# Kernel tuning notes

Measured on AMD Instinct MI355X. Metric: run time of the kernel, lower is better.

The kernel has to match this reference:

```python
import jax, jax.numpy as jnp
from jax import lax
import numpy as np

DN = ('NHWC', 'HWIO', 'NHWC')  # NHWC activations, HWIO kernels (TF layout)
EPS = 1e-3


def setup_inputs() -> dict:
    key = jax.random.key(0)
    ks = jax.random.split(key, 6)
    B, H, W, C = 16, 64, 64, 256
    x = jax.random.normal(ks[0], (B, H, W, C), jnp.float32)
    # per-sample predicted kernels (scaled to keep activations well-conditioned)
    depthwise_kernels = jax.random.normal(ks[1], (B, 3, 3, C, C), jnp.float32) * 0.02
    pointwise_kernels = jax.random.normal(ks[2], (B, 1, 1, C, C), jnp.float32) * 0.06
    biases = jax.random.normal(ks[3], (B, C), jnp.float32) * 0.1
    # shared trailing Conv2D layer params
    conv_w = jax.random.normal(ks[4], (3, 3, C, C), jnp.float32) * 0.02
    conv_b = jnp.zeros((C,), jnp.float32)
    return dict(x=x, depthwise_kernels=depthwise_kernels,
                pointwise_kernels=pointwise_kernels, biases=biases,
                conv_w=conv_w, conv_b=conv_b)


def _instance_norm(x):
    # tf.nn.moments over spatial dims (population variance), eps=0.001
    mean = jnp.mean(x, axis=(1, 2), keepdims=True)
    var = jnp.var(x, axis=(1, 2), keepdims=True)
    return (x - mean) * lax.rsqrt(var + EPS)


def _reflect_pad_hw(x, p=1):
    pad = [(0, 0)] * (x.ndim - 3) + [(p, p), (p, p), (0, 0)]
    return jnp.pad(x, pad, mode='reflect')


def _per_sample_conv(xi, dk, pk, bi):
    # xi: [H,W,C]; dk: [3,3,C,Cm]; pk: [1,1,Cm,Co]; bi: [Co]
    xp = _reflect_pad_hw(xi)[None]  # [1,H+2,W+2,C]
    y = lax.conv_general_dilated(xp, dk, (1, 1), 'VALID', dimension_numbers=DN)
    y = lax.conv_general_dilated(y, pk, (1, 1), 'VALID', dimension_numbers=DN)
    return (y + bi)[0]


def reference(x, depthwise_kernels, pointwise_kernels, biases, conv_w, conv_b):
    x = _instance_norm(x)
    # per-sample kernels -> vmap over batch (replaces tf.map_fn)
    x = jax.vmap(_per_sample_conv)(x, depthwise_kernels, pointwise_kernels, biases)
    # shared Conv2D: reflect pad + VALID conv + bias
    xp = _reflect_pad_hw(x)
    y = lax.conv_general_dilated(xp, conv_w, (1, 1), 'VALID', dimension_numbers=DN)
    return y + conv_b
```

## Files before the change

kernel.cpp:

```cpp
#include <hip/hip_runtime.h>


typedef __bf16 bf16x8 __attribute__((ext_vector_type(8)));
typedef float f32x4 __attribute__((ext_vector_type(4)));

__device__ __forceinline__ float bf2f(unsigned short v) {
    return __uint_as_float(((unsigned int)v) << 16);
}
__device__ __forceinline__ unsigned short f2bf(float f) {
    unsigned int u = __float_as_uint(f);
    unsigned int r = (u + 0x7FFFu + ((u >> 16) & 1u)) >> 16;
    return (unsigned short)r;
}
__device__ __forceinline__ float ldg_elem(const void* p, size_t idx, bool isbf) {
    return isbf ? bf2f(((const unsigned short*)p)[idx]) : ((const float*)p)[idx];
}

__device__ __forceinline__ void gload16(const void* g, void* l) {
    __builtin_amdgcn_global_load_lds(
        (__attribute__((address_space(1))) void*)(unsigned long long)g,
        (__attribute__((address_space(3))) void*)(unsigned long long)l,
        16, 0, 0);
}

#define RAW_BARRIER() do { asm volatile("" ::: "memory"); \
                           __builtin_amdgcn_s_barrier();   \
                           asm volatile("" ::: "memory"); } while (0)

__global__ void detect_dtype(const unsigned short* __restrict__ x, int* __restrict__ flag) {
    __shared__ int wild;
    if (threadIdx.x == 0) wild = 0;
    __syncthreads();
    int cnt = 0;
    for (int i = 0; i < 16; ++i) {
        float a = fabsf(bf2f(x[threadIdx.x * 16 + i]));
        if (!(a < 64.f) || (a != 0.f && a < 1e-5f)) cnt++;
    }
    atomicAdd(&wild, cnt);
    __syncthreads();
    if (threadIdx.x == 0) *flag = (wild > 512) ? 0 : 1;
}

__global__ void norm_partial2(const void* __restrict__ x, const int* __restrict__ flag,
                              float* __restrict__ partS, float* __restrict__ partQ) {
    const bool isbf = (*flag != 0);
    const int b = blockIdx.x, ch = blockIdx.y;
    const int t = threadIdx.x;
    const int l = t & 63;
    const int c4 = l * 4;
    const int sp0 = t >> 6;
    const size_t base = ((size_t)(b * 4096 + ch * 128 + sp0)) * 256 + c4;
    float s[4] = {0.f, 0.f, 0.f, 0.f}, q[4] = {0.f, 0.f, 0.f, 0.f};
    if (isbf) {
        for (int i = 0; i < 32; ++i) {
            const unsigned short* p = (const unsigned short*)x + base + (size_t)i * 1024;
            ushort4 v = *(const ushort4*)p;
            float a[4] = {bf2f(v.x), bf2f(v.y), bf2f(v.z), bf2f(v.w)};
#pragma unroll
            for (int j = 0; j < 4; ++j) { s[j] += a[j]; q[j] += a[j] * a[j]; }
        }
    } else {
        for (int i = 0; i < 32; ++i) {
            float4 v = *(const float4*)((const float*)x + base + (size_t)i * 1024);
            float a[4] = {v.x, v.y, v.z, v.w};
#pragma unroll
            for (int j = 0; j < 4; ++j) { s[j] += a[j]; q[j] += a[j] * a[j]; }
        }
    }
    __shared__ float red[4][64][9];
#pragma unroll
    for (int j = 0; j < 4; ++j) { red[sp0][l][j] = s[j]; red[sp0][l][4 + j] = q[j]; }
    __syncthreads();
    if (t < 64) {
#pragma unroll
        for (int j = 0; j < 4; ++j) {
            float ss = red[0][t][j] + red[1][t][j] + red[2][t][j] + red[3][t][j];
            float qq = red[0][t][4 + j] + red[1][t][4 + j] + red[2][t][4 + j] + red[3][t][4 + j];
            int c = t * 4 + j;
            partS[(b * 32 + ch) * 256 + c] = ss;
            partQ[(b * 32 + ch) * 256 + c] = qq;
        }
    }
}

__global__ void norm_finalize2(const float* __restrict__ partS, const float* __restrict__ partQ,
                               float* __restrict__ mean, float* __restrict__ rstd) {
    const int b = blockIdx.x, c = threadIdx.x;
    float s = 0.f, q = 0.f;
    for (int k = 0; k < 32; ++k) {
        s += partS[(b * 32 + k) * 256 + c];
        q += partQ[(b * 32 + k) * 256 + c];
    }
    float m = s * (1.f / 4096.f);
    float v = q * (1.f / 4096.f) - m * m;
    mean[b * 256 + c] = m;
    rstd[b * 256 + c] = rsqrtf(v + 1e-3f);
}

__global__ void norm_apply(const void* __restrict__ x, const int* __restrict__ flag,
                           const float* __restrict__ mean, const float* __restrict__ rstd,
                           unsigned short* __restrict__ xn) {
    const bool isbf = (*flag != 0);
    size_t e = ((size_t)blockIdx.x * 256 + threadIdx.x) * 8;
    int c0 = (int)(e & 255);
    int bc = (int)(e >> 20) * 256 + c0;
    float v[8];
    if (isbf) {
        uint4 raw = *(const uint4*)((const unsigned short*)x + e);
        unsigned int rr[4] = {raw.x, raw.y, raw.z, raw.w};
#pragma unroll
        for (int i = 0; i < 4; ++i) {
            v[2 * i]     = bf2f((unsigned short)(rr[i] & 0xFFFF));
            v[2 * i + 1] = bf2f((unsigned short)(rr[i] >> 16));
        }
    } else {
        float4 f0 = *(const float4*)((const float*)x + e);
        float4 f1 = *(const float4*)((const float*)x + e + 4);
        v[0] = f0.x; v[1] = f0.y; v[2] = f0.z; v[3] = f0.w;
        v[4] = f1.x; v[5] = f1.y; v[6] = f1.z; v[7] = f1.w;
    }
    unsigned int o[4];
#pragma unroll
    for (int i = 0; i < 4; ++i) {
        unsigned short lo = f2bf((v[2 * i]     - mean[bc + 2 * i])     * rstd[bc + 2 * i]);
        unsigned short hi = f2bf((v[2 * i + 1] - mean[bc + 2 * i + 1]) * rstd[bc + 2 * i + 1]);
        o[i] = (unsigned int)lo | ((unsigned int)hi << 16);
    }
    uint4 out; out.x = o[0]; out.y = o[1]; out.z = o[2]; out.w = o[3];
    *(uint4*)(xn + e) = out;
}

template <bool SCALE>
__global__ void transpose_wk(const void* __restrict__ src, const int* __restrict__ flag,
                             unsigned short* __restrict__ dst,
                             int s_per, long dstBStride, int coStride,
                             const float* __restrict__ rstd) {
    __shared__ unsigned short tile[64][66];
    const bool isbf = (*flag != 0);
    const int sl = blockIdx.x;
    const int b = sl / s_per;
    const size_t dbase = (size_t)b * (size_t)dstBStride + (size_t)(sl % s_per) * 256;
    const int ci0 = blockIdx.y * 64, co0 = blockIdx.z * 64;
    const int t = threadIdx.x;
    const int co4 = (t & 15) * 4;
    const int r0 = t >> 4;
#pragma unroll
    for (int i = 0; i < 4; ++i) {
        int r = r0 + i * 16;
        size_t sidx = (size_t)sl * 65536 + (size_t)(ci0 + r) * 256 + co0 + co4;
        if (isbf) {
            ushort4 v = *(const ushort4*)((const unsigned short*)src + sidx);
            tile[r][co4] = v.x; tile[r][co4 + 1] = v.y;
            tile[r][co4 + 2] = v.z; tile[r][co4 + 3] = v.w;
        } else {
            float4 v = *(const float4*)((const float*)src + sidx);
            tile[r][co4] = f2bf(v.x); tile[r][co4 + 1] = f2bf(v.y);
            tile[r][co4 + 2] = f2bf(v.z); tile[r][co4 + 3] = f2bf(v.w);
        }
    }
    __syncthreads();
    const int cip = (t & 31) * 2;
    const int cob = t >> 5;
    float s0 = 1.f, s1 = 1.f;
    if (SCALE) { s0 = rstd[b * 256 + ci0 + cip]; s1 = rstd[b * 256 + ci0 + cip + 1]; }
#pragma unroll
    for (int i = 0; i < 8; ++i) {
        int co = cob + i * 8;
        unsigned short lo = tile[cip][co], hi = tile[cip + 1][co];
        if (SCALE) { lo = f2bf(bf2f(lo) * s0); hi = f2bf(bf2f(hi) * s1); }
        *(unsigned int*)(dst + dbase + (size_t)(co0 + co) * coStride + ci0 + cip) =
            (unsigned int)lo | ((unsigned int)hi << 16);
    }
}

__global__ void corr_kernel(const unsigned short* __restrict__ dkT,
                            const float* __restrict__ mean,
                            float* __restrict__ negcorr) {
    const int b = blockIdx.x;
    const int lane = threadIdx.x & 63;
    const int co = blockIdx.y * 4 + (threadIdx.x >> 6);
    const unsigned short* wp = dkT + (size_t)(b * 256 + co) * 2304;
    const float* mb = mean + b * 256;
    const int ci0 = (lane & 31) * 8;
    float4 ma = *(const float4*)(mb + ci0);
    float4 mc = *(const float4*)(mb + ci0 + 4);
    float mm[8] = {ma.x, ma.y, ma.z, ma.w, mc.x, mc.y, mc.z, mc.w};
    float sum = 0.f;
#pragma unroll
    for (int c = 0; c < 5; ++c) {
        int k = c * 512 + lane * 8;
        if (k < 2304) {
            uint4 w = *(const uint4*)(wp + k);
            unsigned int wsv[4] = {w.x, w.y, w.z, w.w};
#pragma unroll
            for (int j = 0; j < 4; ++j) {
                sum += bf2f((unsigned short)(wsv[j] & 0xFFFF)) * mm[2 * j];
                sum += bf2f((unsigned short)(wsv[j] >> 16)) * mm[2 * j + 1];
            }
        }
    }
#pragma unroll
    for (int off = 32; off > 0; off >>= 1) sum += __shfl_down(sum, off);
    if (lane == 0) negcorr[b * 256 + co] = -sum;
}

template <bool PER_SAMPLE_W, int BIAS_MODE, bool OUT_F32>
__global__ __launch_bounds__(512, 2) void conv3x3_256(const unsigned short* __restrict__ src,
                                                      const int* __restrict__ flag,
                                                      const unsigned short* __restrict__ wT,
                                                      const void* __restrict__ bias,
                                                      void* __restrict__ dst) {
    constexpr int KTOT = 2304;
    extern __shared__ unsigned short smem[];

    const int t = threadIdx.x;
    const int lane = t & 63;
    const int wave = t >> 6;
    const int wr = wave >> 1;
    const int wc = wave & 1;
    const int bid = blockIdx.x + 16 * blockIdx.z;
    const int b  = (bid & 7) + ((bid >> 3) & 1) * 8;
    const int mt = bid >> 4;
    const int m0 = mt * 256;
    const int R0 = mt * 4;
    const unsigned short* srcB = src + (size_t)b * (4096 * 256);
    const unsigned short* wB = wT + (PER_SAMPLE_W ? (size_t)b * 256 * KTOT : (size_t)0);
    const bool in_bf = (BIAS_MODE >= 2) ? (*flag != 0) : true;

    const int wx = t >> 3;
    const int wg = ((t & 7) ^ (wx & 7)) << 3;
    int wrow[6];
#pragma unroll
    for (int u = 0; u < 6; ++u) {
        int r = R0 - 1 + u;
        wrow[u] = (r < 0) ? 1 : (r > 63 ? 62 : r);
    }
    const unsigned short* winsrc[6];
#pragma unroll
    for (int u = 0; u < 6; ++u)
        winsrc[u] = srcB + ((size_t)wrow[u] * 64 + wx) * 256 + wg;

    const int btrow = t >> 2;
    const int bg = ((t & 3) ^ (btrow & 3)) << 3;
    const unsigned short* bsrc = wB + (size_t)btrow * KTOT + bg;

    auto issueB = [&](int jn) {
        const int cgn = jn / 18, scn = jn % 18;
        const int koff = (scn >> 1) * 256 + cgn * 64 + (scn & 1) * 32;
        unsigned short* bdst = smem + 49152 + (jn % 3) * 8192 + wave * 512;
        gload16(bsrc + koff, bdst);
        gload16(bsrc + (size_t)128 * KTOT + koff, bdst + 4096);
    };

    f32x4 acc[4][8];
#pragma unroll
    for (int i = 0; i < 4; ++i)
#pragma unroll
        for (int j = 0; j < 8; ++j) acc[i][j] = (f32x4){0.f, 0.f, 0.f, 0.f};

    const int fr = lane & 15;
    const int quad = lane >> 4;
    const int cn = wc * 128;
    const int bxor = (quad ^ ((cn + fr) & 3)) << 3;
    int boff[8];
#pragma unroll
    for (int n = 0; n < 8; ++n) boff[n] = (cn + n * 16 + fr) * 32 + bxor;

    auto readB = [&](int jn, int n) -> bf16x8 {
        const unsigned short* slotb = smem + 49152 + (jn % 3) * 8192;
        return *(const bf16x8*)(slotb + boff[n]);
    };
    auto readA = [&](int jn, int mi) -> bf16x8 {
        const int cgn = jn / 18, scn = jn % 18;
        const int tap = scn >> 1, half = scn & 1;
        const int dh = tap / 3 - 1, dw = tap % 3 - 1;
        const unsigned short* A1 = smem + (cgn & 1) * 24576 + (wr + 1 + dh) * 4096;
        int ww = mi * 16 + fr + dw;
        ww = (ww < 0) ? 1 : (ww > 63 ? 62 : ww);
        return *(const bf16x8*)(A1 + ww * 64 + (((half * 4 + quad) ^ (ww & 7)) << 3));
    };

#pragma unroll
    for (int u = 0; u < 6; ++u)
        gload16(winsrc[u], smem + u * 4096 + wave * 512);
    issueB(0);
    issueB(1);
    asm volatile("s_waitcnt vmcnt(0)" ::: "memory");
    RAW_BARRIER();

    bf16x8 afA[4], afB[4], bfr[8];
#pragma unroll
    for (int mi = 0; mi < 4; ++mi) afA[mi] = readA(0, mi);
#pragma unroll
    for (int n = 0; n < 8; ++n) bfr[n] = readB(0, n);

    auto step = [&](int j, bf16x8 (&afc)[4], bf16x8 (&afn)[4]) {
        const int jm = j - 1;
        const bool keep1 = (jm >= 0) && ((jm % 18) >= 8) && ((jm % 18) <= 13) && (jm < 54);
        if (keep1) asm volatile("s_waitcnt vmcnt(1)" ::: "memory");
        else       asm volatile("s_waitcnt vmcnt(0)" ::: "memory");
        RAW_BARRIER();

        const int cgj = j / 18, scj = j % 18;
        if (j + 2 < 72) issueB(j + 2);
        if (cgj < 3 && scj >= 8 && scj <= 13) {
            const int u = scj - 8;
            gload16(winsrc[u] + (cgj + 1) * 64,
                    smem + ((cgj + 1) & 1) * 24576 + u * 4096 + wave * 512);
        }
        if (scj == 0 && j > 0) {
#pragma unroll
            for (int mi = 0; mi < 4; ++mi) afc[mi] = readA(j, mi);
        }
        const bool rdnext = (j < 71);
        __builtin_amdgcn_s_setprio(1);
#pragma unroll
        for (int n = 0; n < 8; ++n) {
#pragma unroll
            for (int mi = 0; mi < 4; ++mi)
                acc[mi][n] = __builtin_amdgcn_mfma_f32_16x16x32_bf16(afc[mi], bfr[n], acc[mi][n], 0, 0, 0);
            if (rdnext) bfr[n] = readB(j + 1, n);
        }
        __builtin_amdgcn_s_setprio(0);
        if (rdnext && ((j + 1) % 18 != 0)) {
#pragma unroll
            for (int mi = 0; mi < 4; ++mi) afn[mi] = readA(j + 1, mi);
        }
    };

    for (int jj = 0; jj < 72; jj += 2) {
        step(jj, afA, afB);
        step(jj + 1, afB, afA);
    }

    const int rbase = quad * 4;
    float bv[8];
#pragma unroll
    for (int n = 0; n < 8; ++n) {
        int nn = cn + n * 16 + fr;
        if (BIAS_MODE == 2)      bv[n] = ldg_elem(bias, b * 256 + nn, in_bf);
        else if (BIAS_MODE == 3) bv[n] = ldg_elem(bias, nn, in_bf);
        else                     bv[n] = 0.f;
    }
#pragma unroll
    for (int m = 0; m < 4; ++m) {
#pragma unroll
        for (int rr = 0; rr < 4; ++rr) {
            int mm = m0 + wr * 64 + m * 16 + rbase + rr;
            size_t rowoff = ((size_t)b * 4096 + mm) * 256;
#pragma unroll
            for (int n = 0; n < 8; ++n) {
                int nn = cn + n * 16 + fr;
                float val = acc[m][n][rr] + bv[n];
                if (OUT_F32) ((float*)dst)[rowoff + nn] = val;
                else         ((unsigned short*)dst)[rowoff + nn] = f2bf(val);
            }
        }
    }
}

template <int KSLICES, bool PER_SAMPLE_W, int BIAS_MODE, bool IS3X3, bool OUT_F32>
__global__ __launch_bounds__(512, 2) void gemm_conv_256(const unsigned short* __restrict__ src,
                                                        const int* __restrict__ flag,
                                                        const unsigned short* __restrict__ wT,
                                                        const void* __restrict__ bias,
                                                        void* __restrict__ dst) {
    constexpr int KTOT = KSLICES * 256;
    constexpr int NKT = KTOT / 64;
    static_assert(NKT >= 2, "pipeline needs >=2 K-tiles");
    extern __shared__ unsigned short smem[];

    const int t = threadIdx.x;
    const int lane = t & 63;
    const int wave = t >> 6;
    const int wr = wave >> 2;
    const int wc = wave & 3;
    const int bid = blockIdx.x + 16 * blockIdx.z;
    const int b  = (bid & 7) + ((bid >> 3) & 1) * 8;
    const int m0 = (bid >> 4) * 256;
    const unsigned short* srcB = src + (size_t)b * (4096 * 256);
    const unsigned short* wB = wT + (PER_SAMPLE_W ? (size_t)b * 256 * KTOT : (size_t)0);
    const bool in_bf = (BIAS_MODE >= 2) ? (*flag != 0) : true;

    const int trow = t >> 3;
    const int tswz = ((t & 7) ^ (trow & 7)) << 3;
    int hU[4], wU[4];
#pragma unroll
    for (int u = 0; u < 4; ++u) {
        int m = m0 + u * 64 + trow;
        hU[u] = m >> 6; wU[u] = m & 63;
    }
    const unsigned short* gBu[4];
#pragma unroll
    for (int u = 0; u < 4; ++u)
        gBu[u] = wB + (size_t)(u * 64 + trow) * KTOT + tswz;

    f32x4 acc[8][4];
#pragma unroll
    for (int i = 0; i < 8; ++i)
#pragma unroll
        for (int j = 0; j < 4; ++j) acc[i][j] = (f32x4){0.f, 0.f, 0.f, 0.f};

    const int fr = lane & 15;
    const int quad = lane >> 4;
    const int fsw = fr & 7;
    const int ks0 = ((quad) ^ fsw) << 3;
    const int ks1 = ((quad + 4) ^ fsw) << 3;
    const int rm = wr * 128;
    const int cn = wc * 64;

#pragma unroll
    for (int kt = 0; kt < 2; ++kt) {
        const int pdh = IS3X3 ? -1 : 0;
        const int pdw = IS3X3 ? -1 : 0;
        const int pchb = (kt & 3) << 6;
        unsigned short* ldsAW = smem + kt * 32768 + wave * 512;
#pragma unroll
        for (int u = 0; u < 4; ++u) {
            int hh = hU[u] + pdh; hh = (hh < 0) ? 1 : (hh > 63 ? 62 : hh);
            int ww = wU[u] + pdw; ww = (ww < 0) ? 1 : (ww > 63 ? 62 : ww);
            gload16(srcB + (size_t)((hh << 6) + ww) * 256 + pchb + tswz, ldsAW + u * 4096);
        }
#pragma unroll
        for (int u = 0; u < 4; ++u)
            gload16(gBu[u] + (size_t)kt * 64, ldsAW + 16384 + u * 4096);
    }
    asm volatile("s_waitcnt vmcnt(8)" ::: "memory");
    RAW_BARRIER();

    bf16x8 af[4][2], bfr[4][2];
    size_t aoff[4];
    int cur_s = -1;

    for (int i = 0; i < NKT; ++i) {
        const int buf = i & 1;
        const unsigned short* As_b = smem + buf * 32768;
        const unsigned short* Bs_b = As_b + 16384;
        unsigned short* ldsAW = smem + buf * 32768 + wave * 512;
        const int kt2 = i + 2;
        const bool st = (kt2 < NKT);

#pragma unroll
        for (int m = 0; m < 4; ++m) {
            const unsigned short* rp = As_b + (rm + m * 16 + fr) * 64;
            af[m][0] = *(const bf16x8*)(rp + ks0);
            af[m][1] = *(const bf16x8*)(rp + ks1);
        }
#pragma unroll
        for (int n = 0; n < 2; ++n) {
            const unsigned short* rp = Bs_b + (cn + n * 16 + fr) * 64;
            bfr[n][0] = *(const bf16x8*)(rp + ks0);
            bfr[n][1] = *(const bf16x8*)(rp + ks1);
        }
        __builtin_amdgcn_s_setprio(1);
#pragma unroll
        for (int m = 0; m < 4; ++m)
#pragma unroll
            for (int n = 0; n < 2; ++n) {
                acc[m][n] = __builtin_amdgcn_mfma_f32_16x16x32_bf16(af[m][0], bfr[n][0], acc[m][n], 0, 0, 0);
                acc[m][n] = __builtin_amdgcn_mfma_f32_16x16x32_bf16(af[m][1], bfr[n][1], acc[m][n], 0, 0, 0);
            }
        __builtin_amdgcn_s_setprio(0);

#pragma unroll
        for (int n = 2; n < 4; ++n) {
            const unsigned short* rp = Bs_b + (cn + n * 16 + fr) * 64;
            bfr[n][0] = *(const bf16x8*)(rp + ks0);
            bfr[n][1] = *(const bf16x8*)(rp + ks1);
        }
        __builtin_amdgcn_s_setprio(1);
#pragma unroll
        for (int m = 0; m < 4; ++m)
#pragma unroll
            for (int n = 2; n < 4; ++n) {
                acc[m][n] = __builtin_amdgcn_mfma_f32_16x16x32_bf16(af[m][0], bfr[n][0], acc[m][n], 0, 0, 0);
                acc[m][n] = __builtin_amdgcn_mfma_f32_16x16x32_bf16(af[m][1], bfr[n][1], acc[m][n], 0, 0, 0);
            }
        __builtin_amdgcn_s_setprio(0);

#pragma unroll
        for (int m = 0; m < 4; ++m) {
            const unsigned short* rp = As_b + (rm + 64 + m * 16 + fr) * 64;
            af[m][0] = *(const bf16x8*)(rp + ks0);
            af[m][1] = *(const bf16x8*)(rp + ks1);
        }
        __builtin_amdgcn_s_setprio(1);
#pragma unroll
        for (int m = 0; m < 4; ++m)
#pragma unroll
            for (int n = 0; n < 4; ++n) {
                acc[4 + m][n] = __builtin_amdgcn_mfma_f32_16x16x32_bf16(af[m][0], bfr[n][0], acc[4 + m][n], 0, 0, 0);
                acc[4 + m][n] = __builtin_amdgcn_mfma_f32_16x16x32_bf16(af[m][1], bfr[n][1], acc[4 + m][n], 0, 0, 0);
            }
        __builtin_amdgcn_s_setprio(0);

        RAW_BARRIER();
        if (st) {
            if (IS3X3) {
                const int s2 = kt2 >> 2;
                if (s2 != cur_s) {
                    cur_s = s2;
                    const int dh2 = s2 / 3 - 1, dw2 = s2 % 3 - 1;
#pragma unroll
                    for (int u = 0; u < 4; ++u) {
                        int hh = hU[u] + dh2; hh = (hh < 0) ? 1 : (hh > 63 ? 62 : hh);
                        int ww = wU[u] + dw2; ww = (ww < 0) ? 1 : (ww > 63 ? 62 : ww);
                        aoff[u] = (size_t)((hh << 6) + ww) * 256 + tswz;
                    }
                }
            } else if (cur_s < 0) {
                cur_s = 0;
#pragma unroll
                for (int u = 0; u < 4; ++u)
                    aoff[u] = (size_t)((hU[u] << 6) + wU[u]) * 256 + tswz;
            }
            const int chb2 = (kt2 & 3) << 6;
#pragma unroll
            for (int u = 0; u < 4; ++u)
                gload16(srcB + aoff[u] + chb2, ldsAW + u * 4096);
#pragma unroll
            for (int u = 0; u < 4; ++u)
                gload16(gBu[u] + (size_t)kt2 * 64, ldsAW + 16384 + u * 4096);
            asm volatile("s_waitcnt vmcnt(8)" ::: "memory");
        } else if (i + 1 < NKT) {
            asm volatile("s_waitcnt vmcnt(0)" ::: "memory");
        }
        RAW_BARRIER();
    }

    const int rbase = quad * 4;
    float bv[4];
#pragma unroll
    for (int n = 0; n < 4; ++n) {
        int nn = cn + n * 16 + fr;
        if (BIAS_MODE == 2)      bv[n] = ldg_elem(bias, b * 256 + nn, in_bf);
        else if (BIAS_MODE == 3) bv[n] = ldg_elem(bias, nn, in_bf);
        else                     bv[n] = 0.f;
    }
#pragma unroll
    for (int m = 0; m < 8; ++m) {
#pragma unroll
        for (int rr = 0; rr < 4; ++rr) {
            int mm = m0 + rm + m * 16 + rbase + rr;
            size_t rowoff = ((size_t)b * 4096 + mm) * 256;
#pragma unroll
            for (int n = 0; n < 4; ++n) {
                int nn = cn + n * 16 + fr;
                float val = acc[m][n][rr] + bv[n];
                if (OUT_F32) ((float*)dst)[rowoff + nn] = val;
                else         ((unsigned short*)dst)[rowoff + nn] = f2bf(val);
            }
        }
    }
}

template <int KSLICES, bool PER_SAMPLE_W, int BIAS_MODE, bool IS3X3, bool SRC_ADAPT, bool OUT_F32>
__global__ __launch_bounds__(256) void gemm_conv(const void* __restrict__ src,
                                                 const int* __restrict__ flag,
                                                 const unsigned short* __restrict__ wT,
                                                 const void* __restrict__ bias,
                                                 void* __restrict__ dst) {
    constexpr int KTOT = KSLICES * 256;
    __shared__ unsigned short As[128][40];
    __shared__ unsigned short Bs[128][40];

    const bool in_bf = (SRC_ADAPT || BIAS_MODE >= 2) ? (*flag != 0) : true;
    const int t = threadIdx.x;
    const int b = blockIdx.z;
    const int m0 = blockIdx.x * 128;
    const int n0 = blockIdx.y * 128;
    const size_t srcOfs = (size_t)b * (4096 * 256);
    const unsigned short* wB = wT + (PER_SAMPLE_W ? (size_t)b * 256 * KTOT : (size_t)0);

    f32x4 acc[4][4];
#pragma unroll
    for (int i = 0; i < 4; ++i)
#pragma unroll
        for (int j = 0; j < 4; ++j) acc[i][j] = (f32x4){0.f, 0.f, 0.f, 0.f};

    const int lane = t & 63;
    const int wave = t >> 6;
    const int rm = (wave >> 1) * 64;
    const int cn = (wave & 1) * 64;
    const int fr = lane & 15;
    const int kg = (lane >> 4) * 8;

    for (int kk = 0; kk < KTOT / 32; ++kk) {
        const int k0 = kk * 32;
        const int s = k0 >> 8;
        const int ci0 = k0 & 255;
        const int dh = IS3X3 ? (s / 3) - 1 : 0;
        const int dw = IS3X3 ? (s % 3) - 1 : 0;
        __syncthreads();
#pragma unroll
        for (int cc = 0; cc < 2; ++cc) {
            int ch = t + cc * 256;
            int r = ch >> 2;
            int ko = (ch & 3) << 3;
            int m = m0 + r;
            int h = m >> 6, w = m & 63;
            if (IS3X3) {
                h += dh; h = (h < 0) ? 1 : (h > 63 ? 62 : h);
                w += dw; w = (w < 0) ? 1 : (w > 63 ? 62 : w);
            }
            size_t eidx = srcOfs + (size_t)((h << 6) + w) * 256 + ci0 + ko;
            if (!SRC_ADAPT || in_bf) {
                uint4 v = *(const uint4*)((const unsigned short*)src + eidx);
                *(uint4*)&As[r][ko] = v;
            } else {
                const float* sf = (const float*)src + eidx;
                float4 f0 = *(const float4*)sf;
                float4 f1 = *(const float4*)(sf + 4);
                uint4 v;
                v.x = (unsigned int)f2bf(f0.x) | ((unsigned int)f2bf(f0.y) << 16);
                v.y = (unsigned int)f2bf(f0.z) | ((unsigned int)f2bf(f0.w) << 16);
                v.z = (unsigned int)f2bf(f1.x) | ((unsigned int)f2bf(f1.y) << 16);
                v.w = (unsigned int)f2bf(f1.z) | ((unsigned int)f2bf(f1.w) << 16);
                *(uint4*)&As[r][ko] = v;
            }
        }
#pragma unroll
        for (int cc = 0; cc < 2; ++cc) {
            int ch = t + cc * 256;
            int n = ch >> 2;
            int ko = (ch & 3) << 3;
            uint4 v = *(const uint4*)(wB + (size_t)(n0 + n) * KTOT + k0 + ko);
            *(uint4*)&Bs[n][ko] = v;
        }
        __syncthreads();

        bf16x8 af[4], bfr[4];
#pragma unroll
        for (int i = 0; i < 4; ++i) af[i] = *(const bf16x8*)&As[rm + i * 16 + fr][kg];
#pragma unroll
        for (int j = 0; j < 4; ++j) bfr[j] = *(const bf16x8*)&Bs[cn + j * 16 + fr][kg];
#pragma unroll
        for (int i = 0; i < 4; ++i)
#pragma unroll
            for (int j = 0; j < 4; ++j)
                acc[i][j] = __builtin_amdgcn_mfma_f32_16x16x32_bf16(af[i], bfr[j], acc[i][j], 0, 0, 0);
    }

    const int rbase = (lane >> 4) * 4;
    const int col = lane & 15;
    float bv[4];
#pragma unroll
    for (int j = 0; j < 4; ++j) {
        int n = n0 + cn + j * 16 + col;
        if (BIAS_MODE == 1)      bv[j] = ((const float*)bias)[b * 256 + n];
        else if (BIAS_MODE == 2) bv[j] = ldg_elem(bias, b * 256 + n, in_bf);
        else if (BIAS_MODE == 3) bv[j] = ldg_elem(bias, n, in_bf);
        else                     bv[j] = 0.f;
    }
#pragma unroll
    for (int i = 0; i < 4; ++i) {
#pragma unroll
        for (int rr = 0; rr < 4; ++rr) {
            int m = m0 + rm + i * 16 + rbase + rr;
            size_t rowoff = ((size_t)b * 4096 + m) * 256;
#pragma unroll
            for (int j = 0; j < 4; ++j) {
                int n = n0 + cn + j * 16 + col;
                float val = acc[i][j][rr] + bv[j];
                if (OUT_F32) ((float*)dst)[rowoff + n] = val;
                else         ((unsigned short*)dst)[rowoff + n] = f2bf(val);
            }
        }
    }
}

extern "C" void kernel_launch(void* const* d_in, const int* in_sizes, int n_in,
                              void* d_out, int out_size, void* d_ws, size_t ws_size,
                              hipStream_t stream) {
    const void* x    = d_in[0];
    const void* dk   = d_in[1];
    const void* pk   = d_in[2];
    const void* bias = d_in[3];
    const void* cw   = d_in[4];
    const void* cb   = d_in[5];

    const size_t NEED_SMALL = 36896768u;
    const size_t NEED_BIG   = 55771136u;
    if (ws_size < NEED_SMALL) return;
    const bool big = (ws_size >= NEED_BIG);

    char* ws = (char*)d_ws;
    int*   flagp   = (int*)ws;
    float* meanp   = (float*)(ws + 1024);
    float* rstdp   = (float*)(ws + 17408);
    float* negcorr = (float*)(ws + 33792);
    unsigned short* pkT = (unsigned short*)(ws + 65536);
    unsigned short* cwT = (unsigned short*)(ws + 2162688);
    unsigned short* dkT = (unsigned short*)(ws + 3342336);
    unsigned short* xn  = (unsigned short*)(ws + 22216704);
    float* partS = (float*)(ws + 22216704);
    float* partQ = (float*)(ws + 22216704 + 524288);
    unsigned short* y2  = big ? xn : dkT;
    unsigned short* y1  = (unsigned short*)d_out;

    hipFuncSetAttribute(reinterpret_cast<const void*>(conv3x3_256<true, 0, false>),
                        hipFuncAttributeMaxDynamicSharedMemorySize, 147456);
    hipFuncSetAttribute(reinterpret_cast<const void*>(conv3x3_256<false, 3, true>),
                        hipFuncAttributeMaxDynamicSharedMemorySize, 147456);
    hipFuncSetAttribute(reinterpret_cast<const void*>(gemm_conv_256<1, true, 2, false, false>),
                        hipFuncAttributeMaxDynamicSharedMemorySize, 131072);

    detect_dtype<<<1, 256, 0, stream>>>((const unsigned short*)x, flagp);
    norm_partial2<<<dim3(16, 32), 256, 0, stream>>>(x, flagp, partS, partQ);
    norm_finalize2<<<16, 256, 0, stream>>>(partS, partQ, meanp, rstdp);

    transpose_wk<false><<<dim3(16, 4, 4), 256, 0, stream>>>(pk, flagp, pkT, 1, 65536L, 256, nullptr);
    transpose_wk<false><<<dim3(9, 4, 4), 256, 0, stream>>>(cw, flagp, cwT, 9, 0L, 2304, nullptr);

    if (big) {
        transpose_wk<false><<<dim3(144, 4, 4), 256, 0, stream>>>(dk, flagp, dkT, 9, 589824L, 2304, nullptr);
        norm_apply<<<8192, 256, 0, stream>>>(x, flagp, meanp, rstdp, xn);
        conv3x3_256<true, 0, false><<<dim3(16, 1, 16), 512, 147456, stream>>>(xn, flagp, dkT, nullptr, y1);
    } else {
        transpose_wk<true><<<dim3(144, 4, 4), 256, 0, stream>>>(dk, flagp, dkT, 9, 589824L, 2304, rstdp);
        corr_kernel<<<dim3(16, 64), 256, 0, stream>>>(dkT, meanp, negcorr);
        gemm_conv<9, true, 1, true, true, false><<<dim3(32, 2, 16), 256, 0, stream>>>(x, flagp, dkT, negcorr, y1);
    }

    gemm_conv_256<1, true, 2, false, false><<<dim3(16, 1, 16), 512, 131072, stream>>>(y1, flagp, pkT, bias, y2);
    conv3x3_256<false, 3, true><<<dim3(16, 1, 16), 512, 147456, stream>>>(y2, flagp, cwT, cb, d_out);
}
```

Before: 351.9 us.

## Restructure conv GEMM main loop with single-buffered A window and 64-K B tiles

Replaces the double-buffered A input window (prefetched during the previous channel group) with a single A buffer that is reloaded synchronously at each channel-group boundary. B weight tiles now cover 64 K values per tap in a 3-slot ring, with half issued on each of two half-steps. The MFMA loop moves from an unrolled two-step lambda with interleaved B reads to a plain loop that runs all MFMAs, then reads the next fragments, then does a full vmcnt(0) wait and barrier every step. This simplifies the code and frees LDS, but it exposes A-load latency at group boundaries and removes the interleaving of LDS reads with MFMAs.

```diff
diff --git a/kernel.cpp b/kernel.cpp
--- a/kernel.cpp
+++ b/kernel.cpp
@@ -239,17 +239,13 @@
 #pragma unroll
     for (int u = 0; u < 6; ++u)
         winsrc[u] = srcB + ((size_t)wrow[u] * 64 + wx) * 256 + wg;
-
-    const int btrow = t >> 2;
-    const int bg = ((t & 3) ^ (btrow & 3)) << 3;
-    const unsigned short* bsrc = wB + (size_t)btrow * KTOT + bg;
-
-    auto issueB = [&](int jn) {
-        const int cgn = jn / 18, scn = jn % 18;
-        const int koff = (scn >> 1) * 256 + cgn * 64 + (scn & 1) * 32;
-        unsigned short* bdst = smem + 49152 + (jn % 3) * 8192 + wave * 512;
-        gload16(bsrc + koff, bdst);
-        gload16(bsrc + (size_t)128 * KTOT + koff, bdst + 4096);
+    const unsigned short* bsrc = wB + (size_t)wx * KTOT + wg;
+
+    auto issueB2 = [&](int T, int u0) {
+        const int koff = (T % 9) * 256 + (T / 9) * 64;
+        unsigned short* bdst = smem + 24576 + (T % 3) * 16384 + wave * 512;
+        gload16(bsrc + (size_t)u0 * 64 * KTOT + koff, bdst + u0 * 4096);
+        gload16(bsrc + (size_t)(u0 + 1) * 64 * KTOT + koff, bdst + (u0 + 1) * 4096);
     };
 
     f32x4 acc[4][8];
@@ -261,76 +257,75 @@
     const int fr = lane & 15;
     const int quad = lane >> 4;
     const int cn = wc * 128;
-    const int bxor = (quad ^ ((cn + fr) & 3)) << 3;
-    int boff[8];
-#pragma unroll
-    for (int n = 0; n < 8; ++n) boff[n] = (cn + n * 16 + fr) * 32 + bxor;
 
     auto readB = [&](int jn, int n) -> bf16x8 {
-        const unsigned short* slotb = smem + 49152 + (jn % 3) * 8192;
-        return *(const bf16x8*)(slotb + boff[n]);
+        const int T = jn >> 1, h = jn & 1;
+        const int co = cn + n * 16 + fr;
+        const unsigned short* p = smem + 24576 + (T % 3) * 16384 + co * 64
+                                  + ((((h << 2) + quad) ^ (co & 7)) << 3);
+        return *(const bf16x8*)p;
     };
     auto readA = [&](int jn, int mi) -> bf16x8 {
-        const int cgn = jn / 18, scn = jn % 18;
-        const int tap = scn >> 1, half = scn & 1;
+        const int T = jn >> 1, h = jn & 1;
+        const int tap = T % 9;
         const int dh = tap / 3 - 1, dw = tap % 3 - 1;
-        const unsigned short* A1 = smem + (cgn & 1) * 24576 + (wr + 1 + dh) * 4096;
         int ww = mi * 16 + fr + dw;
         ww = (ww < 0) ? 1 : (ww > 63 ? 62 : ww);
-        return *(const bf16x8*)(A1 + ww * 64 + (((half * 4 + quad) ^ (ww & 7)) << 3));
+        const unsigned short* p = smem + (wr + 1 + dh) * 4096 + ww * 64
+                                  + ((((h << 2) + quad) ^ (ww & 7)) << 3);
+        return *(const bf16x8*)p;
     };
 
 #pragma unroll
     for (int u = 0; u < 6; ++u)
         gload16(winsrc[u], smem + u * 4096 + wave * 512);
-    issueB(0);
-    issueB(1);
+    issueB2(0, 0); issueB2(0, 2);
+    issueB2(1, 0); issueB2(1, 2);
     asm volatile("s_waitcnt vmcnt(0)" ::: "memory");
     RAW_BARRIER();
 
-    bf16x8 afA[4], afB[4], bfr[8];
-#pragma unroll
-    for (int mi = 0; mi < 4; ++mi) afA[mi] = readA(0, mi);
-#pragma unroll
-    for (int n = 0; n < 8; ++n) bfr[n] = readB(0, n);
-
-    auto step = [&](int j, bf16x8 (&afc)[4], bf16x8 (&afn)[4]) {
-        const int jm = j - 1;
-        const bool keep1 = (jm >= 0) && ((jm % 18) >= 8) && ((jm % 18) <= 13) && (jm < 54);
-        if (keep1) asm volatile("s_waitcnt vmcnt(1)" ::: "memory");
-        else       asm volatile("s_waitcnt vmcnt(0)" ::: "memory");
+    bf16x8 afc[4], bfc[8];
+#pragma unroll
+    for (int mi = 0; mi < 4; ++mi) afc[mi] = readA(0, mi);
+#pragma unroll
+    for (int n = 0; n < 8; ++n) bfc[n] = readB(0, n);
+
+    for (int j = 0; j < 72; ++j) {
+        const int T = j >> 1, h = j & 1;
+        const int scj = j % 18;
+
+        if (scj == 0 && j > 0) {
+            const int cgo = (j / 18) * 64;
+#pragma unroll
+            for (int u = 0; u < 6; ++u)
+                gload16(winsrc[u] + cgo, smem + u * 4096 + wave * 512);
+            asm volatile("s_waitcnt vmcnt(0)" ::: "memory");
+            RAW_BARRIER();
+#pragma unroll
+            for (int mi = 0; mi < 4; ++mi) afc[mi] = readA(j, mi);
+        }
+
+        if (T + 2 < 36) issueB2(T + 2, h * 2);
+
+        __builtin_amdgcn_s_setprio(1);
+#pragma unroll
+        for (int mi = 0; mi < 4; ++mi)
+#pragma unroll
+            for (int n = 0; n < 8; ++n)
+                acc[mi][n] = __builtin_amdgcn_mfma_f32_16x16x32_bf16(afc[mi], bfc[n], acc[mi][n], 0, 0, 0);
+        __builtin_amdgcn_s_setprio(0);
+
+        if (j < 71) {
+#pragma unroll
+            for (int n = 0; n < 8; ++n) bfc[n] = readB(j + 1, n);
+            if ((j + 1) % 18 != 0) {
+#pragma unroll
+                for (int mi = 0; mi < 4; ++mi) afc[mi] = readA(j + 1, mi);
+            }
+        }
+
+        asm volatile("s_waitcnt vmcnt(0)" ::: "memory");
         RAW_BARRIER();
-
-        const int cgj = j / 18, scj = j % 18;
-        if (j + 2 < 72) issueB(j + 2);
-        if (cgj < 3 && scj >= 8 && scj <= 13) {
-            const int u = scj - 8;
-            gload16(winsrc[u] + (cgj + 1) * 64,
-                    smem + ((cgj + 1) & 1) * 24576 + u * 4096 + wave * 512);
-        }
-        if (scj == 0 && j > 0) {
-#pragma unroll
-            for (int mi = 0; mi < 4; ++mi) afc[mi] = readA(j, mi);
-        }
-        const bool rdnext = (j < 71);
-        __builtin_amdgcn_s_setprio(1);
-#pragma unroll
-        for (int n = 0; n < 8; ++n) {
-#pragma unroll
-            for (int mi = 0; mi < 4; ++mi)
-                acc[mi][n] = __builtin_amdgcn_mfma_f32_16x16x32_bf16(afc[mi], bfr[n], acc[mi][n], 0, 0, 0);
-            if (rdnext) bfr[n] = readB(j + 1, n);
-        }
-        __builtin_amdgcn_s_setprio(0);
-        if (rdnext && ((j + 1) % 18 != 0)) {
-#pragma unroll
-            for (int mi = 0; mi < 4; ++mi) afn[mi] = readA(j + 1, mi);
-        }
-    };
-
-    for (int jj = 0; jj < 72; jj += 2) {
-        step(jj, afA, afB);
-        step(jj + 1, afB, afA);
     }
 
     const int rbase = quad * 4;
```

Measured after the change: 353.1 us. No clear change (+0.3%).
